# Kernel tuning notes

Measured on AMD Instinct MI355X. Metric: run time of the kernel, lower is better.

## Reference

```python
import jax, jax.numpy as jnp
import numpy as np

SCALE = 10000.0
PSF = 21          # psf_h == psf_w == psf_d
PAD = PSF // 2    # 10


def setup_inputs() -> dict:
    key = jax.random.key(0)
    k1, k2, k3, k4, k5, k6, k7 = jax.random.split(key, 7)
    N = 8192
    BS, C, H, W, D = 1, 16, 256, 256, 64
    return {
        "psf_raw": jax.random.normal(k1, (N, 1, PSF, PSF, PSF), dtype=jnp.float32),
        "i_val": jax.random.uniform(k2, (N,), dtype=jnp.float32),
        "b": jax.random.randint(k3, (N,), 0, BS, dtype=jnp.int32),
        "ch": jax.random.randint(k4, (N,), 0, C, dtype=jnp.int32),
        "z": jax.random.randint(k5, (N,), 0, H, dtype=jnp.int32),
        "y": jax.random.randint(k6, (N,), 0, W, dtype=jnp.int32),
        "x": jax.random.randint(k7, (N,), 0, D, dtype=jnp.int32),
        "BS": BS, "C": C, "H": H, "W": W, "D": D,
    }


def reference(psf_raw, i_val, b, ch, z, y, x, BS, C, H, W, D):
    # 1) clamp_min_(psf, 0)
    psf = jnp.maximum(psf_raw, 0.0)
    # 2) normalize by per-emitter max over spatial dims
    psf = psf / psf.max(axis=(2, 3, 4), keepdims=True)
    # 3) scale by clamped intensity
    psf = psf * jnp.maximum(i_val, 0.0)[:, None, None, None, None]
    # 4) reshape (N, 1, p, p, p) -> (N, p, p, p) as in _place_psf
    psf = psf.reshape(-1, PSF, PSF, PSF)

    # scatter-add each patch into the padded volume; slice start in the padded
    # array is exactly the original coordinate (z_idx - pad == z).
    Hp, Wp, Dp = H + 2 * PAD, W + 2 * PAD, D + 2 * PAD
    iz = jnp.arange(PSF, dtype=jnp.int32)[:, None, None]   # (p,1,1)
    iy = jnp.arange(PSF, dtype=jnp.int32)[None, :, None]   # (1,p,1)
    ix = jnp.arange(PSF, dtype=jnp.int32)[None, None, :]   # (1,1,p)
    off = b * C + ch                                        # (N,)
    lin = (((off[:, None, None, None] * Hp + (z[:, None, None, None] + iz)) * Wp
            + (y[:, None, None, None] + iy)) * Dp
           + (x[:, None, None, None] + ix))                 # (N,p,p,p)

    flat = jnp.zeros(BS * C * Hp * Wp * Dp, dtype=psf.dtype)
    flat = flat.at[lin.reshape(-1)].add(psf.reshape(-1))
    vol = flat.reshape(BS, C, Hp, Wp, Dp)
    xsim = vol[:, :, PAD:PAD + H, PAD:PAD + W, PAD:PAD + D]
    return SCALE * xsim
```

## Files before the change

kernel.cpp:

```cpp
#include <hip/hip_runtime.h>

#define SCALE_F 10000.0f
#define PSF 21
#define PAD 10
#define PSF3 9261
#define NTILES 16384

#define META_OFF 0
#define CNT_OFF  131072
#define SCAN_OFF 196608
#define CUR_OFF  262144
#define LIST_OFF 327680

__global__ __launch_bounds__(256) void psf_scale_fill_kernel(
    const float* __restrict__ psf_raw,
    const float* __restrict__ i_val,
    const int* __restrict__ bArr, const int* __restrict__ chArr,
    const int* __restrict__ zArr, const int* __restrict__ yArr,
    const int* __restrict__ xArr,
    int4* __restrict__ meta,
    int*  __restrict__ cnt,
    int*  __restrict__ list,
    int cap)
{
    const int n   = blockIdx.x;
    const int tid = threadIdx.x;
    const float* p = psf_raw + (size_t)n * PSF3;

    const int peel = (4 - (n & 3)) & 3;
    float m = 0.0f;
    if (tid < peel) m = fmaxf(m, p[tid]);
    const float4* p4 = (const float4*)(p + peel);
    const int nq = (PSF3 - peel) >> 2;
    for (int k = tid; k < nq; k += 256) {
        float4 q = p4[k];
        m = fmaxf(m, fmaxf(fmaxf(q.x, q.y), fmaxf(q.z, q.w)));
    }
    const int rem = (PSF3 - peel) & 3;
    if (tid < rem) m = fmaxf(m, p[PSF3 - rem + tid]);

#pragma unroll
    for (int off = 32; off > 0; off >>= 1)
        m = fmaxf(m, __shfl_down(m, off, 64));

    __shared__ float smax[4];
    if ((tid & 63) == 0) smax[tid >> 6] = m;
    __syncthreads();
    if (tid == 0) {
        float mm = fmaxf(fmaxf(smax[0], smax[1]), fmaxf(smax[2], smax[3]));
        float sc = (mm > 0.0f) ? SCALE_F * fmaxf(i_val[n], 0.0f) / mm : 0.0f;
        int z0 = zArr[n] - PAD, y0 = yArr[n] - PAD, x0 = xArr[n] - PAD;
        meta[n] = make_int4(z0, y0, x0, __float_as_int(sc));
        int c = bArr[n] * 16 + chArr[n];
        int tzlo = max(z0, 0) >> 3, tzhi = min(z0 + 20, 255) >> 3;
        int tylo = max(y0, 0) >> 3, tyhi = min(y0 + 20, 255) >> 3;
        if (cap > 0) {
            for (int tz = tzlo; tz <= tzhi; ++tz)
                for (int ty = tylo; ty <= tyhi; ++ty) {
                    int t = c * 1024 + tz * 32 + ty;
                    int pos = atomicAdd(&cnt[t], 1);
                    if (pos < cap) list[t * cap + pos] = n;
                }
        } else {
            for (int tz = tzlo; tz <= tzhi; ++tz)
                for (int ty = tylo; ty <= tyhi; ++ty)
                    atomicAdd(&cnt[c * 1024 + tz * 32 + ty], 1);
        }
    }
}

__global__ __launch_bounds__(256) void scan_kernel(
    const int4* __restrict__ cnt4, int4* __restrict__ off4, int4* __restrict__ cur4)
{
    const int t = threadIdx.x;
    int4 v[16];
#pragma unroll
    for (int i = 0; i < 16; ++i) v[i] = cnt4[t * 16 + i];
    int sum = 0;
#pragma unroll
    for (int i = 0; i < 16; ++i) sum += v[i].x + v[i].y + v[i].z + v[i].w;

    const int lane = t & 63, w = t >> 6;
    int s = sum;
#pragma unroll
    for (int d = 1; d < 64; d <<= 1) {
        int u = __shfl_up(s, d, 64);
        if (lane >= d) s += u;
    }
    __shared__ int wsum[4];
    if (lane == 63) wsum[w] = s;
    __syncthreads();
    int base = 0;
    for (int i = 0; i < w; ++i) base += wsum[i];
    int run = base + s - sum;

#pragma unroll
    for (int i = 0; i < 16; ++i) {
        int4 o;
        o.x = run; run += v[i].x;
        o.y = run; run += v[i].y;
        o.z = run; run += v[i].z;
        o.w = run; run += v[i].w;
        off4[t * 16 + i] = o;
        cur4[t * 16 + i] = o;
    }
}

__global__ __launch_bounds__(256) void fill_kernel(
    const int* __restrict__ bArr, const int* __restrict__ chArr,
    const int* __restrict__ zArr, const int* __restrict__ yArr,
    int* __restrict__ cursor, int* __restrict__ list, int N)
{
    int n = blockIdx.x * 256 + threadIdx.x;
    if (n >= N) return;
    int c = bArr[n] * 16 + chArr[n];
    int z0 = zArr[n] - PAD, y0 = yArr[n] - PAD;
    int tzlo = max(z0, 0) >> 3, tzhi = min(z0 + 20, 255) >> 3;
    int tylo = max(y0, 0) >> 3, tyhi = min(y0 + 20, 255) >> 3;
    for (int tz = tzlo; tz <= tzhi; ++tz)
        for (int ty = tylo; ty <= tyhi; ++ty) {
            int pos = atomicAdd(&cursor[c * 1024 + tz * 32 + ty], 1);
            list[pos] = n;
        }
}

__global__ __launch_bounds__(256) void gather_kernel(
    const float* __restrict__ psf_raw,
    const int4* __restrict__ meta,
    const int* __restrict__ off, const int* __restrict__ cnt,
    const int* __restrict__ list,
    float* __restrict__ out,
    int cap)
{
    const int tile = blockIdx.x;
    const int ty = tile & 31;
    const int tz = (tile >> 5) & 31;
    const int c  = tile >> 10;
    const int t  = threadIdx.x;
    const int x    = t & 63;
    const int ysub = t >> 6;
    const int zbase = tz * 8;
    const int ybase = ty * 8;

    float acc0[8] = {};
    float acc1[8] = {};

    int o, cn;
    if (cap > 0) { o = tile * cap; cn = min(cnt[tile], cap); }
    else         { o = off[tile];  cn = cnt[tile]; }

    int  nnext = (cn > 0) ? list[o] : 0;
    int4 mnext = (cn > 0) ? meta[nnext] : make_int4(0, 0, 0, 0);

    for (int i = 0; i < cn; ++i) {
        const int  n  = __builtin_amdgcn_readfirstlane(nnext);
        const int4 mt = mnext;
        const int  nj = list[o + min(i + 1, cn - 1)];
        nnext = nj;
        mnext = meta[nj];

        const int z0 = __builtin_amdgcn_readfirstlane(mt.x);
        const int y0 = __builtin_amdgcn_readfirstlane(mt.y);
        const int x0 = __builtin_amdgcn_readfirstlane(mt.z);
        const float sc = __int_as_float(__builtin_amdgcn_readfirstlane(mt.w));

        const int dx  = x - x0;
        const float wsc = ((unsigned)dx < 21u) ? sc : 0.0f;
        const int dxc = min(max(dx, 0), 20);

        const int dy0 = ybase + ysub - y0;
        const int dy1 = dy0 + 4;
        const int a0 = __any((unsigned)dy0 < 21u);
        const int a1 = __any((unsigned)dy1 < 21u);
        const int row0 = dy0 * 21 + dxc;
        const int row1 = dy1 * 21 + dxc;
        const float* pb = psf_raw + (size_t)n * PSF3;

        if (a0 & a1) {
#pragma unroll
            for (int zi = 0; zi < 8; ++zi) {
                const int dz = zbase + zi - z0;
                const int zo = min(max(dz, 0), 20) * 441;
                const float w = ((unsigned)dz < 21u) ? wsc : 0.0f;
                acc0[zi] += w * fmaxf(pb[zo + row0], 0.0f);
                acc1[zi] += w * fmaxf(pb[zo + row1], 0.0f);
            }
        } else if (a0) {
#pragma unroll
            for (int zi = 0; zi < 8; ++zi) {
                const int dz = zbase + zi - z0;
                const int zo = min(max(dz, 0), 20) * 441;
                const float w = ((unsigned)dz < 21u) ? wsc : 0.0f;
                acc0[zi] += w * fmaxf(pb[zo + row0], 0.0f);
            }
        } else if (a1) {
#pragma unroll
            for (int zi = 0; zi < 8; ++zi) {
                const int dz = zbase + zi - z0;
                const int zo = min(max(dz, 0), 20) * 441;
                const float w = ((unsigned)dz < 21u) ? wsc : 0.0f;
                acc1[zi] += w * fmaxf(pb[zo + row1], 0.0f);
            }
        }
    }

    const size_t outbase = (((size_t)c * 256 + zbase) * 256 + ybase) * 64 + x;
#pragma unroll
    for (int zi = 0; zi < 8; ++zi) {
        __builtin_nontemporal_store(acc0[zi],
            &out[outbase + (size_t)zi * (256 * 64) + (size_t)ysub * 64]);
        __builtin_nontemporal_store(acc1[zi],
            &out[outbase + (size_t)zi * (256 * 64) + (size_t)(ysub + 4) * 64]);
    }
}

extern "C" void kernel_launch(void* const* d_in, const int* in_sizes, int n_in,
                              void* d_out, int out_size, void* d_ws, size_t ws_size,
                              hipStream_t stream) {
    const float* psf_raw = (const float*)d_in[0];
    const float* i_val   = (const float*)d_in[1];
    const int*   bArr    = (const int*)d_in[2];
    const int*   chArr   = (const int*)d_in[3];
    const int*   zArr    = (const int*)d_in[4];
    const int*   yArr    = (const int*)d_in[5];
    const int*   xArr    = (const int*)d_in[6];
    float* out = (float*)d_out;

    const int N = in_sizes[1];

    char* ws = (char*)d_ws;
    int4*  meta   = (int4*)(ws + META_OFF);
    int*   cnt    = (int*)(ws + CNT_OFF);
    int*   off    = (int*)(ws + SCAN_OFF);
    int*   cursor = (int*)(ws + CUR_OFF);
    int*   list   = (int*)(ws + LIST_OFF);

    size_t avail = (ws_size > LIST_OFF) ? (ws_size - LIST_OFF) : 0;
    size_t cap_s = avail / ((size_t)NTILES * sizeof(int));
    int cap = (cap_s >= 64) ? 64 : (int)cap_s;
    if (cap < 24) cap = 0;

    hipMemsetAsync(cnt, 0, NTILES * sizeof(int), stream);

    psf_scale_fill_kernel<<<N, 256, 0, stream>>>(psf_raw, i_val, bArr, chArr,
                                                 zArr, yArr, xArr, meta, cnt, list, cap);
    if (cap == 0) {
        scan_kernel<<<1, 256, 0, stream>>>((const int4*)cnt, (int4*)off, (int4*)cursor);
        fill_kernel<<<(N + 255) / 256, 256, 0, stream>>>(bArr, chArr, zArr, yArr,
                                                         cursor, list, N);
    }
    gather_kernel<<<NTILES, 256, 0, stream>>>(psf_raw, meta, off, cnt, list, out, cap);
}
```

Before: 186.8 us.

## Pre-scale PSFs into fp16 workspace copy for the gather pass

The first kernel now keeps each emitter's PSF in registers, then writes a clamped, normalised and intensity-scaled fp16 copy into workspace. The gather kernel reads these half-precision values instead of the raw fp32 PSF, which halves the bytes it gathers and drops the per-element clamp. This adds a full extra write pass of about 150MB of fp16 data and lowers precision, since values up to 10000 are stored in fp16. The path only runs when the workspace is large enough, otherwise it falls back to the fp32 path.

```diff
diff --git a/kernel.cpp b/kernel.cpp
--- a/kernel.cpp
+++ b/kernel.cpp
@@ -1,17 +1,24 @@
 #include <hip/hip_runtime.h>
+#include <hip/hip_fp16.h>
 
 #define SCALE_F 10000.0f
 #define PSF 21
 #define PAD 10
 #define PSF3 9261
+#define PSF3P 9280
 #define NTILES 16384
+#define CAP 64
+
+typedef float f32x4 __attribute__((ext_vector_type(4)));
 
 #define META_OFF 0
 #define CNT_OFF  131072
 #define SCAN_OFF 196608
 #define CUR_OFF  262144
 #define LIST_OFF 327680
-
+#define PSC_OFF  4521984
+
+template<bool F16>
 __global__ __launch_bounds__(256) void psf_scale_fill_kernel(
     const float* __restrict__ psf_raw,
     const float* __restrict__ i_val,
@@ -21,23 +28,35 @@
     int4* __restrict__ meta,
     int*  __restrict__ cnt,
     int*  __restrict__ list,
-    int cap)
+    int cap,
+    __half* __restrict__ pscaled)
 {
     const int n   = blockIdx.x;
     const int tid = threadIdx.x;
     const float* p = psf_raw + (size_t)n * PSF3;
 
     const int peel = (4 - (n & 3)) & 3;
-    float m = 0.0f;
-    if (tid < peel) m = fmaxf(m, p[tid]);
-    const float4* p4 = (const float4*)(p + peel);
-    const int nq = (PSF3 - peel) >> 2;
-    for (int k = tid; k < nq; k += 256) {
-        float4 q = p4[k];
-        m = fmaxf(m, fmaxf(fmaxf(q.x, q.y), fmaxf(q.z, q.w)));
-    }
+    const f32x4* p4 = (const f32x4*)(p + peel);
+    const int nq  = (PSF3 - peel) >> 2;
     const int rem = (PSF3 - peel) & 3;
-    if (tid < rem) m = fmaxf(m, p[PSF3 - rem + tid]);
+
+    float head = 0.0f, tailv = 0.0f;
+    if (tid < peel) head  = p[tid];
+    if (tid < rem)  tailv = p[PSF3 - rem + tid];
+
+    f32x4 q[10];
+    float m = fmaxf(fmaxf(head, tailv), 0.0f);
+#pragma unroll
+    for (int j = 0; j < 10; ++j) {
+        const int k = tid + (j << 8);
+        if (j < 9 || k < nq) {
+            f32x4 v = __builtin_nontemporal_load(p4 + k);
+            q[j] = v;
+            m = fmaxf(m, fmaxf(fmaxf(v.x, v.y), fmaxf(v.z, v.w)));
+        } else {
+            q[j] = (f32x4)(0.0f);
+        }
+    }
 
 #pragma unroll
     for (int off = 32; off > 0; off >>= 1)
@@ -46,9 +65,31 @@
     __shared__ float smax[4];
     if ((tid & 63) == 0) smax[tid >> 6] = m;
     __syncthreads();
+    const float mm = fmaxf(fmaxf(smax[0], smax[1]), fmaxf(smax[2], smax[3]));
+    const float sc = (mm > 0.0f) ? SCALE_F * fmaxf(i_val[n], 0.0f) / mm : 0.0f;
+
+    if (F16) {
+        __half* pb = pscaled + (size_t)n * PSF3P;
+        if (tid < peel)
+            pb[tid - peel] = __float2half_rn(sc * fmaxf(head, 0.0f));
+        if (tid < rem)
+            pb[PSF3 - rem + tid - peel] = __float2half_rn(sc * fmaxf(tailv, 0.0f));
+        ushort4* pq = (ushort4*)pb;
+#pragma unroll
+        for (int j = 0; j < 10; ++j) {
+            const int k = tid + (j << 8);
+            if (j < 9 || k < nq) {
+                ushort4 u;
+                u.x = __half_as_ushort(__float2half_rn(sc * fmaxf(q[j].x, 0.0f)));
+                u.y = __half_as_ushort(__float2half_rn(sc * fmaxf(q[j].y, 0.0f)));
+                u.z = __half_as_ushort(__float2half_rn(sc * fmaxf(q[j].z, 0.0f)));
+                u.w = __half_as_ushort(__float2half_rn(sc * fmaxf(q[j].w, 0.0f)));
+                pq[k] = u;
+            }
+        }
+    }
+
     if (tid == 0) {
-        float mm = fmaxf(fmaxf(smax[0], smax[1]), fmaxf(smax[2], smax[3]));
-        float sc = (mm > 0.0f) ? SCALE_F * fmaxf(i_val[n], 0.0f) / mm : 0.0f;
         int z0 = zArr[n] - PAD, y0 = yArr[n] - PAD, x0 = xArr[n] - PAD;
         meta[n] = make_int4(z0, y0, x0, __float_as_int(sc));
         int c = bArr[n] * 16 + chArr[n];
@@ -124,8 +165,10 @@
         }
 }
 
+template<bool F16>
 __global__ __launch_bounds__(256) void gather_kernel(
     const float* __restrict__ psf_raw,
+    const __half* __restrict__ pscaled,
     const int4* __restrict__ meta,
     const int* __restrict__ off, const int* __restrict__ cnt,
     const int* __restrict__ list,
@@ -165,7 +208,7 @@
         const float sc = __int_as_float(__builtin_amdgcn_readfirstlane(mt.w));
 
         const int dx  = x - x0;
-        const float wsc = ((unsigned)dx < 21u) ? sc : 0.0f;
+        const float wsc = ((unsigned)dx < 21u) ? (F16 ? 1.0f : sc) : 0.0f;
         const int dxc = min(max(dx, 0), 20);
 
         const int dy0 = ybase + ysub - y0;
@@ -174,7 +217,9 @@
         const int a1 = __any((unsigned)dy1 < 21u);
         const int row0 = dy0 * 21 + dxc;
         const int row1 = dy1 * 21 + dxc;
-        const float* pb = psf_raw + (size_t)n * PSF3;
+
+        const float*  pbf = psf_raw + (size_t)n * PSF3;
+        const __half* pbh = pscaled + (size_t)n * PSF3P - ((4 - (n & 3)) & 3);
 
         if (a0 & a1) {
 #pragma unroll
@@ -182,8 +227,10 @@
                 const int dz = zbase + zi - z0;
                 const int zo = min(max(dz, 0), 20) * 441;
                 const float w = ((unsigned)dz < 21u) ? wsc : 0.0f;
-                acc0[zi] += w * fmaxf(pb[zo + row0], 0.0f);
-                acc1[zi] += w * fmaxf(pb[zo + row1], 0.0f);
+                float v0 = F16 ? __half2float(pbh[zo + row0]) : fmaxf(pbf[zo + row0], 0.0f);
+                float v1 = F16 ? __half2float(pbh[zo + row1]) : fmaxf(pbf[zo + row1], 0.0f);
+                acc0[zi] += w * v0;
+                acc1[zi] += w * v1;
             }
         } else if (a0) {
 #pragma unroll
@@ -191,7 +238,8 @@
                 const int dz = zbase + zi - z0;
                 const int zo = min(max(dz, 0), 20) * 441;
                 const float w = ((unsigned)dz < 21u) ? wsc : 0.0f;
-                acc0[zi] += w * fmaxf(pb[zo + row0], 0.0f);
+                float v0 = F16 ? __half2float(pbh[zo + row0]) : fmaxf(pbf[zo + row0], 0.0f);
+                acc0[zi] += w * v0;
             }
         } else if (a1) {
 #pragma unroll
@@ -199,7 +247,8 @@
                 const int dz = zbase + zi - z0;
                 const int zo = min(max(dz, 0), 20) * 441;
                 const float w = ((unsigned)dz < 21u) ? wsc : 0.0f;
-                acc1[zi] += w * fmaxf(pb[zo + row1], 0.0f);
+                float v1 = F16 ? __half2float(pbh[zo + row1]) : fmaxf(pbf[zo + row1], 0.0f);
+                acc1[zi] += w * v1;
             }
         }
     }
@@ -229,25 +278,44 @@
     const int N = in_sizes[1];
 
     char* ws = (char*)d_ws;
-    int4*  meta   = (int4*)(ws + META_OFF);
-    int*   cnt    = (int*)(ws + CNT_OFF);
-    int*   off    = (int*)(ws + SCAN_OFF);
-    int*   cursor = (int*)(ws + CUR_OFF);
-    int*   list   = (int*)(ws + LIST_OFF);
-
-    size_t avail = (ws_size > LIST_OFF) ? (ws_size - LIST_OFF) : 0;
-    size_t cap_s = avail / ((size_t)NTILES * sizeof(int));
-    int cap = (cap_s >= 64) ? 64 : (int)cap_s;
-    if (cap < 24) cap = 0;
-
-    hipMemsetAsync(cnt, 0, NTILES * sizeof(int), stream);
-
-    psf_scale_fill_kernel<<<N, 256, 0, stream>>>(psf_raw, i_val, bArr, chArr,
-                                                 zArr, yArr, xArr, meta, cnt, list, cap);
+    int4*   meta    = (int4*)(ws + META_OFF);
+    int*    cnt     = (int*)(ws + CNT_OFF);
+    int*    offp    = (int*)(ws + SCAN_OFF);
+    int*    cursor  = (int*)(ws + CUR_OFF);
+    int*    list    = (int*)(ws + LIST_OFF);
+    __half* pscaled = (__half*)(ws + PSC_OFF) + 16;
+
+    const size_t psc_need = (size_t)PSC_OFF + 64 + (size_t)N * PSF3P * 2;
+    bool f16 = (ws_size >= psc_need);
+    int cap;
+    if (ws_size >= (size_t)LIST_OFF + (size_t)CAP * NTILES * 4) {
+        cap = CAP;
+    } else {
+        size_t avail = (ws_size > LIST_OFF) ? ws_size - LIST_OFF : 0;
+        size_t cap_s = avail / ((size_t)NTILES * sizeof(int));
+        cap = (cap_s >= 24) ? (int)((cap_s < 64) ? cap_s : 64) : 0;
+    }
+    if (cap == 0) f16 = false;
+
+    (void)hipMemsetAsync(cnt, 0, NTILES * sizeof(int), stream);
+
+    if (f16)
+        psf_scale_fill_kernel<true><<<N, 256, 0, stream>>>(psf_raw, i_val, bArr, chArr,
+            zArr, yArr, xArr, meta, cnt, list, cap, pscaled);
+    else
+        psf_scale_fill_kernel<false><<<N, 256, 0, stream>>>(psf_raw, i_val, bArr, chArr,
+            zArr, yArr, xArr, meta, cnt, list, cap, pscaled);
+
     if (cap == 0) {
-        scan_kernel<<<1, 256, 0, stream>>>((const int4*)cnt, (int4*)off, (int4*)cursor);
+        scan_kernel<<<1, 256, 0, stream>>>((const int4*)cnt, (int4*)offp, (int4*)cursor);
         fill_kernel<<<(N + 255) / 256, 256, 0, stream>>>(bArr, chArr, zArr, yArr,
                                                          cursor, list, N);
     }
-    gather_kernel<<<NTILES, 256, 0, stream>>>(psf_raw, meta, off, cnt, list, out, cap);
-}
+
+    if (f16)
+        gather_kernel<true><<<NTILES, 256, 0, stream>>>(psf_raw, pscaled, meta,
+            offp, cnt, list, out, cap);
+    else
+        gather_kernel<false><<<NTILES, 256, 0, stream>>>(psf_raw, pscaled, meta,
+            offp, cnt, list, out, cap);
+}
```

After: 168.3 us, median of 2. -9.9%, faster.
